# Kernel optimization log

Hardware: AMD Instinct MI355X
Metric: run time of the kernel (lower is better)

## Reference

```python
import jax, jax.numpy as jnp
import numpy as np

N = 50000       # num nodes
E = 800000      # num edges (avg degree 16)
D_IN = 128
D_H = 128
D_LAT = 64
BN_EPS = 1e-5


def _glorot(key, fan_in, fan_out):
    return jax.random.normal(key, (fan_in, fan_out), jnp.float32) / np.sqrt(fan_in).astype(np.float32)


def setup_inputs() -> dict:
    key = jax.random.key(0)
    ks = jax.random.split(key, 8)
    x = jax.random.normal(ks[0], (N, D_IN), jnp.float32)
    edge_index = jax.random.randint(ks[1], (2, E), 0, N)  # row 0 = src, row 1 = dst
    return {
        "x": x,
        "edge_index": edge_index,
        "W0": _glorot(ks[2], D_IN, D_H),
        "W1": _glorot(ks[3], D_H, D_H),
        "W_mu": _glorot(ks[4], D_H, D_LAT),
        "W_logvar": _glorot(ks[5], D_H, D_LAT),
        "gamma0": jnp.ones((D_H,), jnp.float32),
        "beta0": jnp.zeros((D_H,), jnp.float32),
        "gamma1": jnp.ones((D_H,), jnp.float32),
        "beta1": jnp.zeros((D_H,), jnp.float32),
    }


def _gcn_conv(h, W, src, dst, dinv):
    # Standard GCN with self-loops: D^{-1/2}(A+I)D^{-1/2} (X W)
    m = h @ W                                   # [N, out]
    coef = (dinv[src] * dinv[dst])[:, None]     # [E, 1]
    out = jax.ops.segment_sum(m[src] * coef, dst, num_segments=N)
    return out + m * (dinv * dinv)[:, None]     # self-loop contribution


def _batchnorm(h, gamma, beta):
    mean = jnp.mean(h, axis=0)
    var = jnp.var(h, axis=0)
    return (h - mean) * jax.lax.rsqrt(var + BN_EPS) * gamma + beta


def reference(x, edge_index, W0, W1, W_mu, W_logvar, gamma0, beta0, gamma1, beta1):
    # decoder_type='graph', augment_type=None, used_edge_weight=False,
    # use_FCencoder=False, num_domains=1; dropout is identity in reference.
    src, dst = edge_index[0], edge_index[1]
    deg = jax.ops.segment_sum(jnp.ones((E,), x.dtype), dst, num_segments=N) + 1.0
    dinv = jax.lax.rsqrt(deg)

    h = _gcn_conv(x, W0, src, dst, dinv)
    h = jax.nn.relu(_batchnorm(h, gamma0, beta0))
    h = _gcn_conv(h, W1, src, dst, dinv)
    h = jax.nn.relu(_batchnorm(h, gamma1, beta1))

    z_mean = _gcn_conv(h, W_mu, src, dst, dinv)
    z_log_std = _gcn_conv(h, W_logvar, src, dst, dinv)
    return (z_mean, z_log_std)
```

## Files before the change

kernel.cpp:

```cpp
#include <hip/hip_runtime.h>
#include <hip/hip_bf16.h>


using short8 = __attribute__((ext_vector_type(8))) short;
using f32x4  = __attribute__((ext_vector_type(4))) float;

static __device__ __forceinline__ unsigned short f2bf(float f) {
    __hip_bfloat16 h = __float2bfloat16(f);
    return *reinterpret_cast<unsigned short*>(&h);
}
static __device__ __forceinline__ float bf_lo(unsigned int u) {
    return __uint_as_float(u << 16);
}
static __device__ __forceinline__ float bf_hi(unsigned int u) {
    return __uint_as_float(u & 0xffff0000u);
}
static __device__ __forceinline__ float bf2f(unsigned short u) {
    return __uint_as_float((unsigned int)u << 16);
}

__global__ __launch_bounds__(256)
void deg_count(const int* __restrict__ ei, int* __restrict__ cnt, int E_) {
    int e = blockIdx.x * 256 + threadIdx.x;
    if (e < E_) atomicAdd(&cnt[ei[E_ + e]], 1);
}

__global__ __launch_bounds__(1024)
void scan_blocks(const int* __restrict__ cnt, float* __restrict__ dinv,
                 int* __restrict__ rowptr, int* __restrict__ partials, int n) {
    __shared__ int ls[1024];
    int tid = threadIdx.x;
    int i = blockIdx.x * 1024 + tid;
    int v = (i < n) ? cnt[i] : 0;
    if (i < n) dinv[i] = rsqrtf((float)v + 1.0f);
    ls[tid] = v;
    __syncthreads();
    #pragma unroll
    for (int off = 1; off < 1024; off <<= 1) {
        int t = (tid >= off) ? ls[tid - off] : 0;
        __syncthreads();
        ls[tid] += t;
        __syncthreads();
    }
    if (i < n) rowptr[i] = ls[tid] - v;
    if (tid == 1023) partials[blockIdx.x] = ls[1023];
}

__global__ __launch_bounds__(1024)
void scan_partials(int* __restrict__ partials, int* __restrict__ rowptr_n,
                   int nb) {
    __shared__ int ls[1024];
    int tid = threadIdx.x;
    int v = (tid < nb) ? partials[tid] : 0;
    ls[tid] = v;
    __syncthreads();
    #pragma unroll
    for (int off = 1; off < 1024; off <<= 1) {
        int t = (tid >= off) ? ls[tid - off] : 0;
        __syncthreads();
        ls[tid] += t;
        __syncthreads();
    }
    if (tid < nb) partials[tid] = ls[tid] - v;
    if (tid == 1023) *rowptr_n = ls[1023];
}

__global__ __launch_bounds__(256)
void scan_add(int* __restrict__ rowptr, int* __restrict__ gcursor,
              const int* __restrict__ partials, int n) {
    int i = blockIdx.x * 256 + threadIdx.x;
    if (i < n) {
        int v = rowptr[i] + partials[i >> 10];
        rowptr[i] = v;
        if ((i & 127) == 0) gcursor[i >> 7] = v;
    }
}

#define BCHUNK 4096
__global__ __launch_bounds__(256)
void bin_edges(const int* __restrict__ ei, const float* __restrict__ dinv,
               int* __restrict__ gcursor, uint2* __restrict__ binned, int E_) {
    __shared__ int hist[512];
    __shared__ int gbase[512];
    __shared__ int cur[512];
    const int tid = threadIdx.x;
    const int e0 = blockIdx.x * BCHUNK;

    #pragma unroll
    for (int q = 0; q < 2; ++q) hist[q * 256 + tid] = 0;
    __syncthreads();

    for (int i = tid; i < BCHUNK; i += 256) {
        int e = e0 + i;
        if (e < E_) atomicAdd(&hist[ei[E_ + e] >> 7], 1);
    }
    __syncthreads();

    #pragma unroll
    for (int q = 0; q < 2; ++q) {
        int b = q * 256 + tid;
        int c = hist[b];
        gbase[b] = c ? atomicAdd(&gcursor[b], c) : 0;
        cur[b] = 0;
    }
    __syncthreads();

    for (int i = tid; i < BCHUNK; i += 256) {
        int e = e0 + i;
        if (e >= E_) continue;
        int s = ei[e], d = ei[E_ + e];
        float coef = dinv[s] * dinv[d];
        unsigned int cb = (__float_as_uint(coef) + 0x8000u) >> 16;
        unsigned int entry = ((unsigned int)s << 15) | (cb & 0x7fffu);
        int b = d >> 7;
        int p = gbase[b] + atomicAdd(&cur[b], 1);
        binned[p] = make_uint2(entry, (unsigned int)(d & 127));
    }
}

__global__ __launch_bounds__(256)
void place_edges(const uint2* __restrict__ binned, const int* __restrict__ rowptr,
                 unsigned int* __restrict__ csr, int n) {
    __shared__ int cur[128];
    const int tid = threadIdx.x;
    const int n0 = blockIdx.x * 128;
    const int nn = min(128, n - n0);
    if (tid < nn) cur[tid] = rowptr[n0 + tid];
    __syncthreads();
    const int beg = rowptr[n0];
    const int end = rowptr[min(n0 + 128, n)];
    for (int i = beg + tid; i < end; i += 256) {
        uint2 v = binned[i];
        int p = atomicAdd(&cur[v.y], 1);
        csr[p] = v.x;
    }
}

template<bool XBF, bool FUSE_BN, bool SPLIT_W>
__global__ __launch_bounds__(256)
void gemm_mfma(const void* __restrict__ Xv, const float* __restrict__ Wa,
               const float* __restrict__ Wb, const float* __restrict__ sc,
               const float* __restrict__ sh, unsigned short* __restrict__ Y,
               int nRows) {
    __shared__ unsigned short wt[128 * 128];

    const int tid = threadIdx.x;

    #pragma unroll
    for (int it = 0; it < 16; ++it) {
        int flat4 = it * 256 + tid;
        int k  = flat4 >> 5;
        int c0 = (flat4 & 31) * 4;
        const float* srcp;
        if (!SPLIT_W) srcp = Wa + k * 128 + c0;
        else          srcp = (c0 < 64) ? (Wa + k * 64 + c0)
                                       : (Wb + k * 64 + (c0 - 64));
        float4 v = *(const float4*)srcp;
        float vv[4] = {v.x, v.y, v.z, v.w};
        #pragma unroll
        for (int j = 0; j < 4; ++j) {
            int c = c0 + j;
            wt[c * 128 + (k ^ ((c & 7) << 3))] = f2bf(vv[j]);
        }
    }
    __syncthreads();

    const int lane = tid & 63;
    const int wv   = tid >> 6;
    const int lm   = lane & 15;
    const int lg   = lane >> 4;
    const int row0 = blockIdx.x * 128 + wv * 32;

    f32x4 acc[2][8] = {};

    #pragma unroll
    for (int ks = 0; ks < 4; ++ks) {
        const int k0 = ks * 32 + lg * 8;

        short8 a[2];
        #pragma unroll
        for (int mf = 0; mf < 2; ++mf) {
            int r = row0 + mf * 16 + lm;
            if (r < nRows) {
                if (XBF) {
                    a[mf] = *(const short8*)((const unsigned short*)Xv +
                                             (size_t)r * 128 + k0);
                    if (FUSE_BN) {
                        float4 s0 = *(const float4*)(sc + k0);
                        float4 s1 = *(const float4*)(sc + k0 + 4);
                        float4 h0 = *(const float4*)(sh + k0);
                        float4 h1 = *(const float4*)(sh + k0 + 4);
                        float sv[8] = {s0.x, s0.y, s0.z, s0.w, s1.x, s1.y, s1.z, s1.w};
                        float hv[8] = {h0.x, h0.y, h0.z, h0.w, h1.x, h1.y, h1.z, h1.w};
                        #pragma unroll
                        for (int j = 0; j < 8; ++j) {
                            float v = bf2f((unsigned short)a[mf][j]);
                            v = fmaxf(v * sv[j] + hv[j], 0.f);
                            a[mf][j] = (short)f2bf(v);
                        }
                    }
                } else {
                    const float* xp = (const float*)Xv + (size_t)r * 128 + k0;
                    float4 p0 = *(const float4*)xp;
                    float4 p1 = *(const float4*)(xp + 4);
                    float pv[8] = {p0.x, p0.y, p0.z, p0.w, p1.x, p1.y, p1.z, p1.w};
                    #pragma unroll
                    for (int j = 0; j < 8; ++j) a[mf][j] = (short)f2bf(pv[j]);
                }
            } else {
                a[mf] = short8{};
            }
        }

        #pragma unroll
        for (int f = 0; f < 8; ++f) {
            int c = f * 16 + lm;
            short8 b = *(const short8*)&wt[c * 128 + (k0 ^ ((c & 7) << 3))];
            acc[0][f] = __builtin_amdgcn_mfma_f32_16x16x32_bf16(a[0], b, acc[0][f], 0, 0, 0);
            acc[1][f] = __builtin_amdgcn_mfma_f32_16x16x32_bf16(a[1], b, acc[1][f], 0, 0, 0);
        }
    }

    #pragma unroll
    for (int mf = 0; mf < 2; ++mf) {
        #pragma unroll
        for (int reg = 0; reg < 4; ++reg) {
            int r = row0 + mf * 16 + lg * 4 + reg;
            if (r >= nRows) continue;
            #pragma unroll
            for (int f = 0; f < 8; ++f)
                Y[(size_t)r * 128 + f * 16 + lm] = f2bf(acc[mf][f][reg]);
        }
    }
}

template<bool TO_OUT>
__global__ __launch_bounds__(256)
void gather_bf(const unsigned short* __restrict__ M,
               const int* __restrict__ rowptr,
               const unsigned int* __restrict__ csr,
               const float* __restrict__ dinv, void* __restrict__ O, int n) {
    int wid  = (blockIdx.x * 256 + threadIdx.x) >> 6;
    int lane = threadIdx.x & 63;
    if (wid >= n) return;
    const unsigned int* m2 = (const unsigned int*)M;

    float di = dinv[wid];
    unsigned int su = m2[(size_t)wid * 64 + lane];
    float c = di * di;
    float ax0 = bf_lo(su) * c, ay0 = bf_hi(su) * c;
    float ax1 = 0.f, ay1 = 0.f, ax2 = 0.f, ay2 = 0.f, ax3 = 0.f, ay3 = 0.f;
    float ax4 = 0.f, ay4 = 0.f, ax5 = 0.f, ay5 = 0.f, ax6 = 0.f, ay6 = 0.f;
    float ax7 = 0.f, ay7 = 0.f;

    int beg = __builtin_amdgcn_readfirstlane(rowptr[wid]);
    int end = __builtin_amdgcn_readfirstlane(rowptr[wid + 1]);

    int k = beg;
    for (; k + 7 < end; k += 8) {
        unsigned int e0 = csr[k],     e1 = csr[k + 1];
        unsigned int e2 = csr[k + 2], e3 = csr[k + 3];
        unsigned int e4 = csr[k + 4], e5 = csr[k + 5];
        unsigned int e6 = csr[k + 6], e7 = csr[k + 7];
        unsigned int u0 = m2[(size_t)(e0 >> 15) * 64 + lane];
        unsigned int u1 = m2[(size_t)(e1 >> 15) * 64 + lane];
        unsigned int u2 = m2[(size_t)(e2 >> 15) * 64 + lane];
        unsigned int u3 = m2[(size_t)(e3 >> 15) * 64 + lane];
        unsigned int u4 = m2[(size_t)(e4 >> 15) * 64 + lane];
        unsigned int u5 = m2[(size_t)(e5 >> 15) * 64 + lane];
        unsigned int u6 = m2[(size_t)(e6 >> 15) * 64 + lane];
        unsigned int u7 = m2[(size_t)(e7 >> 15) * 64 + lane];
        float w0 = __uint_as_float((e0 & 0x7fffu) << 16);
        float w1 = __uint_as_float((e1 & 0x7fffu) << 16);
        float w2 = __uint_as_float((e2 & 0x7fffu) << 16);
        float w3 = __uint_as_float((e3 & 0x7fffu) << 16);
        float w4 = __uint_as_float((e4 & 0x7fffu) << 16);
        float w5 = __uint_as_float((e5 & 0x7fffu) << 16);
        float w6 = __uint_as_float((e6 & 0x7fffu) << 16);
        float w7 = __uint_as_float((e7 & 0x7fffu) << 16);
        ax0 += w0 * bf_lo(u0); ay0 += w0 * bf_hi(u0);
        ax1 += w1 * bf_lo(u1); ay1 += w1 * bf_hi(u1);
        ax2 += w2 * bf_lo(u2); ay2 += w2 * bf_hi(u2);
        ax3 += w3 * bf_lo(u3); ay3 += w3 * bf_hi(u3);
        ax4 += w4 * bf_lo(u4); ay4 += w4 * bf_hi(u4);
        ax5 += w5 * bf_lo(u5); ay5 += w5 * bf_hi(u5);
        ax6 += w6 * bf_lo(u6); ay6 += w6 * bf_hi(u6);
        ax7 += w7 * bf_lo(u7); ay7 += w7 * bf_hi(u7);
    }
    for (; k < end; ++k) {
        unsigned int e0 = csr[k];
        unsigned int u0 = m2[(size_t)(e0 >> 15) * 64 + lane];
        float w0 = __uint_as_float((e0 & 0x7fffu) << 16);
        ax0 += w0 * bf_lo(u0); ay0 += w0 * bf_hi(u0);
    }
    float ax = ((ax0 + ax1) + (ax2 + ax3)) + ((ax4 + ax5) + (ax6 + ax7));
    float ay = ((ay0 + ay1) + (ay2 + ay3)) + ((ay4 + ay5) + (ay6 + ay7));

    if (!TO_OUT) {
        unsigned int o = (unsigned int)f2bf(ax) | ((unsigned int)f2bf(ay) << 16);
        ((unsigned int*)O)[(size_t)wid * 64 + lane] = o;
    } else {
        float* Of = (float*)O;
        float* dst = (lane < 32)
            ? Of + (size_t)wid * 64 + 2 * lane
            : Of + (size_t)n * 64 + (size_t)wid * 64 + 2 * (lane - 32);
        *(float2*)dst = make_float2(ax, ay);
    }
}

__global__ __launch_bounds__(256)
void bn_stats(const unsigned short* __restrict__ H, float* __restrict__ stats,
              const float* __restrict__ gamma, const float* __restrict__ beta,
              float* __restrict__ sc, float* __restrict__ sh,
              unsigned int* __restrict__ ticket, int n) {
    const uint4* h4 = (const uint4*)H;
    const int tid = threadIdx.x;
    const int cg = tid & 15;
    const int rg = tid >> 4;
    float s[8] = {}, q[8] = {};
    for (int r = blockIdx.x * 16 + rg; r < n; r += gridDim.x * 16) {
        uint4 u = h4[(size_t)r * 16 + cg];
        float v[8] = {bf_lo(u.x), bf_hi(u.x), bf_lo(u.y), bf_hi(u.y),
                      bf_lo(u.z), bf_hi(u.z), bf_lo(u.w), bf_hi(u.w)};
        #pragma unroll
        for (int j = 0; j < 8; ++j) { s[j] += v[j]; q[j] += v[j] * v[j]; }
    }
    __shared__ float ls[256][17];
    #pragma unroll
    for (int j = 0; j < 8; ++j) { ls[tid][j] = s[j]; ls[tid][8 + j] = q[j]; }
    __syncthreads();
    if (tid < 128) {
        int cgrp = tid >> 3, j = tid & 7;
        float S = 0.f, Q = 0.f;
        #pragma unroll
        for (int g = 0; g < 16; ++g) {
            S += ls[(g << 4) | cgrp][j];
            Q += ls[(g << 4) | cgrp][8 + j];
        }
        atomicAdd(&stats[tid], S);
        atomicAdd(&stats[128 + tid], Q);
    }
    __syncthreads();
    __shared__ int lastFlag;
    if (tid == 0) {
        __threadfence();
        unsigned int t = atomicAdd(ticket, 1u);
        lastFlag = (t == gridDim.x - 1);
    }
    __syncthreads();
    if (lastFlag && tid < 128) {
        float Ssum = __hip_atomic_load(&stats[tid], __ATOMIC_RELAXED,
                                       __HIP_MEMORY_SCOPE_AGENT);
        float Qsum = __hip_atomic_load(&stats[128 + tid], __ATOMIC_RELAXED,
                                       __HIP_MEMORY_SCOPE_AGENT);
        float inv_n = 1.0f / (float)n;
        float mean = Ssum * inv_n;
        float var  = Qsum * inv_n - mean * mean;
        float sv = rsqrtf(var + 1e-5f) * gamma[tid];
        sc[tid] = sv;
        sh[tid] = beta[tid] - mean * sv;
    }
}

extern "C" void kernel_launch(void* const* d_in, const int* in_sizes, int n_in,
                              void* d_out, int out_size, void* d_ws, size_t ws_size,
                              hipStream_t stream) {
    const float* x    = (const float*)d_in[0];
    const int*   ei   = (const int*)d_in[1];
    const float* W0   = (const float*)d_in[2];
    const float* W1   = (const float*)d_in[3];
    const float* Wmu  = (const float*)d_in[4];
    const float* Wlog = (const float*)d_in[5];
    const float* g0   = (const float*)d_in[6];
    const float* b0   = (const float*)d_in[7];
    const float* g1   = (const float*)d_in[8];
    const float* b1   = (const float*)d_in[9];

    const int N_ = in_sizes[0] / 128;
    const int E_ = in_sizes[1] / 2;
    float* out = (float*)d_out;

    char* w = (char*)d_ws;
    auto carve = [&](size_t bytes) {
        char* p = w;
        w += (bytes + 255) & ~(size_t)255;
        return p;
    };
    int*   cnt     = (int*)  carve((size_t)N_ * 4);
    float* stats0  = (float*)carve(256 * 4);
    float* stats1  = (float*)carve(256 * 4);
    unsigned int* ticket0 = (unsigned int*)carve(256);
    unsigned int* ticket1 = (unsigned int*)carve(256);
    char*  zend    = w;
    float* dinv    = (float*)carve((size_t)N_ * 4);
    int*   rowptr  = (int*)  carve((size_t)(N_ + 1) * 4);
    int*   gcursor = (int*)  carve(512 * 4);
    int*   partials= (int*)  carve(1024 * 4);
    unsigned int* csr = (unsigned int*)carve((size_t)E_ * 4);
    uint2* binned  = (uint2*)carve((size_t)E_ * 8);
    float* sc0     = (float*)carve(128 * 4);
    float* sh0     = (float*)carve(128 * 4);
    float* sc1     = (float*)carve(128 * 4);
    float* sh1     = (float*)carve(128 * 4);
    unsigned short* Mbf = (unsigned short*)carve((size_t)N_ * 128 * 2);
    unsigned short* Hb  = (unsigned short*)carve((size_t)N_ * 128 * 2);

    const int gGemm = (N_ + 127) / 128;
    const int gGath = (N_ * 64 + 255) / 256;
    const int nb    = (N_ + 1023) / 1024;
    const int nbk   = (N_ + 127) / 128;
    const int gBin  = (E_ + BCHUNK - 1) / BCHUNK;

    hipMemsetAsync(cnt, 0, (size_t)(zend - (char*)cnt), stream);
    deg_count<<<(E_ + 255) / 256, 256, 0, stream>>>(ei, cnt, E_);
    scan_blocks<<<nb, 1024, 0, stream>>>(cnt, dinv, rowptr, partials, N_);
    scan_partials<<<1, 1024, 0, stream>>>(partials, rowptr + N_, nb);
    scan_add<<<(N_ + 255) / 256, 256, 0, stream>>>(rowptr, gcursor, partials, N_);
    bin_edges<<<gBin, 256, 0, stream>>>(ei, dinv, gcursor, binned, E_);
    place_edges<<<nbk, 256, 0, stream>>>(binned, rowptr, csr, N_);

    gemm_mfma<false, false, false><<<gGemm, 256, 0, stream>>>(
        x, W0, nullptr, nullptr, nullptr, Mbf, N_);
    gather_bf<false><<<gGath, 256, 0, stream>>>(Mbf, rowptr, csr, dinv, Hb, N_);
    bn_stats<<<512, 256, 0, stream>>>(Hb, stats0, g0, b0, sc0, sh0, ticket0, N_);

    gemm_mfma<true, true, false><<<gGemm, 256, 0, stream>>>(
        Hb, W1, nullptr, sc0, sh0, Mbf, N_);
    gather_bf<false><<<gGath, 256, 0, stream>>>(Mbf, rowptr, csr, dinv, Hb, N_);
    bn_stats<<<512, 256, 0, stream>>>(Hb, stats1, g1, b1, sc1, sh1, ticket1, N_);

    gemm_mfma<true, true, true><<<gGemm, 256, 0, stream>>>(
        Hb, Wmu, Wlog, sc1, sh1, Mbf, N_);
    gather_bf<true><<<gGath, 256, 0, stream>>>(Mbf, rowptr, csr, dinv, out, N_);
}
```

Measured before the change: 259.8 us.

## Fuse BatchNorm statistics into gather kernel with sharded atomic accumulators

Merges the bn_stats pass into the aggregation kernel: each block reduces sum and sum-of-squares of its 4 rows in shared memory and atomically adds them into one of 16 shadow stat buffers, and the last block to finish folds these into scale and shift. This avoids re-reading the hidden activations and removes two launches. The cost is 12500 blocks each issuing 256 float atomics, contended across only 16 buffers, and a statistics order that is no longer deterministic. deg_count is also changed to read destinations as int4 with four atomics per thread.

```diff
diff --git a/kernel.cpp b/kernel.cpp
--- a/kernel.cpp
+++ b/kernel.cpp
@@ -21,8 +21,15 @@
 
 __global__ __launch_bounds__(256)
 void deg_count(const int* __restrict__ ei, int* __restrict__ cnt, int E_) {
-    int e = blockIdx.x * 256 + threadIdx.x;
-    if (e < E_) atomicAdd(&cnt[ei[E_ + e]], 1);
+    int i = blockIdx.x * 256 + threadIdx.x;
+    int nq = E_ >> 2;
+    const int4* d4 = (const int4*)(ei + E_);
+    if (i < nq) {
+        int4 v = d4[i];
+        atomicAdd(&cnt[v.x], 1); atomicAdd(&cnt[v.y], 1);
+        atomicAdd(&cnt[v.z], 1); atomicAdd(&cnt[v.w], 1);
+    }
+    if (i < (E_ & 3)) atomicAdd(&cnt[ei[E_ + nq * 4 + i]], 1);
 }
 
 __global__ __launch_bounds__(1024)
@@ -234,28 +241,12 @@
     }
 }
 
-template<bool TO_OUT>
-__global__ __launch_bounds__(256)
-void gather_bf(const unsigned short* __restrict__ M,
-               const int* __restrict__ rowptr,
-               const unsigned int* __restrict__ csr,
-               const float* __restrict__ dinv, void* __restrict__ O, int n) {
-    int wid  = (blockIdx.x * 256 + threadIdx.x) >> 6;
-    int lane = threadIdx.x & 63;
-    if (wid >= n) return;
-    const unsigned int* m2 = (const unsigned int*)M;
-
-    float di = dinv[wid];
-    unsigned int su = m2[(size_t)wid * 64 + lane];
-    float c = di * di;
-    float ax0 = bf_lo(su) * c, ay0 = bf_hi(su) * c;
+static __device__ __forceinline__ void gather_row(
+        const unsigned int* __restrict__ m2, const unsigned int* __restrict__ csr,
+        int beg, int end, int lane, float& ax, float& ay) {
     float ax1 = 0.f, ay1 = 0.f, ax2 = 0.f, ay2 = 0.f, ax3 = 0.f, ay3 = 0.f;
     float ax4 = 0.f, ay4 = 0.f, ax5 = 0.f, ay5 = 0.f, ax6 = 0.f, ay6 = 0.f;
     float ax7 = 0.f, ay7 = 0.f;
-
-    int beg = __builtin_amdgcn_readfirstlane(rowptr[wid]);
-    int end = __builtin_amdgcn_readfirstlane(rowptr[wid + 1]);
-
     int k = beg;
     for (; k + 7 < end; k += 8) {
         unsigned int e0 = csr[k],     e1 = csr[k + 1];
@@ -278,7 +269,7 @@
         float w5 = __uint_as_float((e5 & 0x7fffu) << 16);
         float w6 = __uint_as_float((e6 & 0x7fffu) << 16);
         float w7 = __uint_as_float((e7 & 0x7fffu) << 16);
-        ax0 += w0 * bf_lo(u0); ay0 += w0 * bf_hi(u0);
+        ax  += w0 * bf_lo(u0); ay  += w0 * bf_hi(u0);
         ax1 += w1 * bf_lo(u1); ay1 += w1 * bf_hi(u1);
         ax2 += w2 * bf_lo(u2); ay2 += w2 * bf_hi(u2);
         ax3 += w3 * bf_lo(u3); ay3 += w3 * bf_hi(u3);
@@ -291,54 +282,56 @@
         unsigned int e0 = csr[k];
         unsigned int u0 = m2[(size_t)(e0 >> 15) * 64 + lane];
         float w0 = __uint_as_float((e0 & 0x7fffu) << 16);
-        ax0 += w0 * bf_lo(u0); ay0 += w0 * bf_hi(u0);
-    }
-    float ax = ((ax0 + ax1) + (ax2 + ax3)) + ((ax4 + ax5) + (ax6 + ax7));
-    float ay = ((ay0 + ay1) + (ay2 + ay3)) + ((ay4 + ay5) + (ay6 + ay7));
-
-    if (!TO_OUT) {
+        ax += w0 * bf_lo(u0); ay += w0 * bf_hi(u0);
+    }
+    ax = ((ax + ax1) + (ax2 + ax3)) + ((ax4 + ax5) + (ax6 + ax7));
+    ay = ((ay + ay1) + (ay2 + ay3)) + ((ay4 + ay5) + (ay6 + ay7));
+}
+
+__global__ __launch_bounds__(256)
+void gather_stats(const unsigned short* __restrict__ M,
+                  const int* __restrict__ rowptr,
+                  const unsigned int* __restrict__ csr,
+                  const float* __restrict__ dinv, unsigned int* __restrict__ O,
+                  float* __restrict__ stats,
+                  const float* __restrict__ gamma, const float* __restrict__ beta,
+                  float* __restrict__ sc, float* __restrict__ sh,
+                  unsigned int* __restrict__ ticket, int n) {
+    const int tid  = threadIdx.x;
+    const int wv   = tid >> 6;
+    const int lane = tid & 63;
+    const int wid  = blockIdx.x * 4 + wv;
+    const unsigned int* m2 = (const unsigned int*)M;
+
+    float ax = 0.f, ay = 0.f;
+    if (wid < n) {
+        float di = dinv[wid];
+        unsigned int su = m2[(size_t)wid * 64 + lane];
+        float c = di * di;
+        ax = bf_lo(su) * c; ay = bf_hi(su) * c;
+        int beg = __builtin_amdgcn_readfirstlane(rowptr[wid]);
+        int end = __builtin_amdgcn_readfirstlane(rowptr[wid + 1]);
+        gather_row(m2, csr, beg, end, lane, ax, ay);
         unsigned int o = (unsigned int)f2bf(ax) | ((unsigned int)f2bf(ay) << 16);
-        ((unsigned int*)O)[(size_t)wid * 64 + lane] = o;
-    } else {
-        float* Of = (float*)O;
-        float* dst = (lane < 32)
-            ? Of + (size_t)wid * 64 + 2 * lane
-            : Of + (size_t)n * 64 + (size_t)wid * 64 + 2 * (lane - 32);
-        *(float2*)dst = make_float2(ax, ay);
-    }
-}
-
-__global__ __launch_bounds__(256)
-void bn_stats(const unsigned short* __restrict__ H, float* __restrict__ stats,
-              const float* __restrict__ gamma, const float* __restrict__ beta,
-              float* __restrict__ sc, float* __restrict__ sh,
-              unsigned int* __restrict__ ticket, int n) {
-    const uint4* h4 = (const uint4*)H;
-    const int tid = threadIdx.x;
-    const int cg = tid & 15;
-    const int rg = tid >> 4;
-    float s[8] = {}, q[8] = {};
-    for (int r = blockIdx.x * 16 + rg; r < n; r += gridDim.x * 16) {
-        uint4 u = h4[(size_t)r * 16 + cg];
-        float v[8] = {bf_lo(u.x), bf_hi(u.x), bf_lo(u.y), bf_hi(u.y),
-                      bf_lo(u.z), bf_hi(u.z), bf_lo(u.w), bf_hi(u.w)};
-        #pragma unroll
-        for (int j = 0; j < 8; ++j) { s[j] += v[j]; q[j] += v[j] * v[j]; }
-    }
-    __shared__ float ls[256][17];
-    #pragma unroll
-    for (int j = 0; j < 8; ++j) { ls[tid][j] = s[j]; ls[tid][8 + j] = q[j]; }
-    __syncthreads();
-    if (tid < 128) {
-        int cgrp = tid >> 3, j = tid & 7;
-        float S = 0.f, Q = 0.f;
-        #pragma unroll
-        for (int g = 0; g < 16; ++g) {
-            S += ls[(g << 4) | cgrp][j];
-            Q += ls[(g << 4) | cgrp][8 + j];
-        }
-        atomicAdd(&stats[tid], S);
-        atomicAdd(&stats[128 + tid], Q);
+        O[(size_t)wid * 64 + lane] = o;
+    }
+
+    __shared__ float ls[4][64][4];
+    ls[wv][lane][0] = ax;       ls[wv][lane][1] = ay;
+    ls[wv][lane][2] = ax * ax;  ls[wv][lane][3] = ay * ay;
+    __syncthreads();
+    if (tid < 64) {
+        float sx = 0.f, sy = 0.f, qx = 0.f, qy = 0.f;
+        #pragma unroll
+        for (int g = 0; g < 4; ++g) {
+            sx += ls[g][tid][0]; sy += ls[g][tid][1];
+            qx += ls[g][tid][2]; qy += ls[g][tid][3];
+        }
+        float* shadow = stats + (blockIdx.x & 15) * 256;
+        atomicAdd(&shadow[2 * tid],       sx);
+        atomicAdd(&shadow[2 * tid + 1],   sy);
+        atomicAdd(&shadow[128 + 2 * tid], qx);
+        atomicAdd(&shadow[129 + 2 * tid], qy);
     }
     __syncthreads();
     __shared__ int lastFlag;
@@ -349,17 +342,46 @@
     }
     __syncthreads();
     if (lastFlag && tid < 128) {
-        float Ssum = __hip_atomic_load(&stats[tid], __ATOMIC_RELAXED,
-                                       __HIP_MEMORY_SCOPE_AGENT);
-        float Qsum = __hip_atomic_load(&stats[128 + tid], __ATOMIC_RELAXED,
-                                       __HIP_MEMORY_SCOPE_AGENT);
+        float S = 0.f, Q = 0.f;
+        #pragma unroll
+        for (int g = 0; g < 16; ++g) {
+            S += __hip_atomic_load(&stats[g * 256 + tid], __ATOMIC_RELAXED,
+                                   __HIP_MEMORY_SCOPE_AGENT);
+            Q += __hip_atomic_load(&stats[g * 256 + 128 + tid], __ATOMIC_RELAXED,
+                                   __HIP_MEMORY_SCOPE_AGENT);
+        }
         float inv_n = 1.0f / (float)n;
-        float mean = Ssum * inv_n;
-        float var  = Qsum * inv_n - mean * mean;
+        float mean = S * inv_n;
+        float var  = Q * inv_n - mean * mean;
         float sv = rsqrtf(var + 1e-5f) * gamma[tid];
         sc[tid] = sv;
         sh[tid] = beta[tid] - mean * sv;
     }
+}
+
+__global__ __launch_bounds__(256)
+void gather_out(const unsigned short* __restrict__ M,
+                const int* __restrict__ rowptr,
+                const unsigned int* __restrict__ csr,
+                const float* __restrict__ dinv, float* __restrict__ O, int n) {
+    int wid  = (blockIdx.x * 256 + threadIdx.x) >> 6;
+    int lane = threadIdx.x & 63;
+    if (wid >= n) return;
+    const unsigned int* m2 = (const unsigned int*)M;
+
+    float di = dinv[wid];
+    unsigned int su = m2[(size_t)wid * 64 + lane];
+    float c = di * di;
+    float ax = bf_lo(su) * c, ay = bf_hi(su) * c;
+
+    int beg = __builtin_amdgcn_readfirstlane(rowptr[wid]);
+    int end = __builtin_amdgcn_readfirstlane(rowptr[wid + 1]);
+    gather_row(m2, csr, beg, end, lane, ax, ay);
+
+    float* dst = (lane < 32)
+        ? O + (size_t)wid * 64 + 2 * lane
+        : O + (size_t)n * 64 + (size_t)wid * 64 + 2 * (lane - 32);
+    *(float2*)dst = make_float2(ax, ay);
 }
 
 extern "C" void kernel_launch(void* const* d_in, const int* in_sizes, int n_in,
@@ -387,8 +409,8 @@
         return p;
     };
     int*   cnt     = (int*)  carve((size_t)N_ * 4);
-    float* stats0  = (float*)carve(256 * 4);
-    float* stats1  = (float*)carve(256 * 4);
+    float* stats0  = (float*)carve(16 * 256 * 4);
+    float* stats1  = (float*)carve(16 * 256 * 4);
     unsigned int* ticket0 = (unsigned int*)carve(256);
     unsigned int* ticket1 = (unsigned int*)carve(256);
     char*  zend    = w;
@@ -406,13 +428,13 @@
     unsigned short* Hb  = (unsigned short*)carve((size_t)N_ * 128 * 2);
 
     const int gGemm = (N_ + 127) / 128;
-    const int gGath = (N_ * 64 + 255) / 256;
+    const int gGath = (N_ + 3) / 4;
     const int nb    = (N_ + 1023) / 1024;
     const int nbk   = (N_ + 127) / 128;
     const int gBin  = (E_ + BCHUNK - 1) / BCHUNK;
 
     hipMemsetAsync(cnt, 0, (size_t)(zend - (char*)cnt), stream);
-    deg_count<<<(E_ + 255) / 256, 256, 0, stream>>>(ei, cnt, E_);
+    deg_count<<<((E_ >> 2) + 255) / 256, 256, 0, stream>>>(ei, cnt, E_);
     scan_blocks<<<nb, 1024, 0, stream>>>(cnt, dinv, rowptr, partials, N_);
     scan_partials<<<1, 1024, 0, stream>>>(partials, rowptr + N_, nb);
     scan_add<<<(N_ + 255) / 256, 256, 0, stream>>>(rowptr, gcursor, partials, N_);
@@ -421,15 +443,16 @@
 
     gemm_mfma<false, false, false><<<gGemm, 256, 0, stream>>>(
         x, W0, nullptr, nullptr, nullptr, Mbf, N_);
-    gather_bf<false><<<gGath, 256, 0, stream>>>(Mbf, rowptr, csr, dinv, Hb, N_);
-    bn_stats<<<512, 256, 0, stream>>>(Hb, stats0, g0, b0, sc0, sh0, ticket0, N_);
+    gather_stats<<<gGath, 256, 0, stream>>>(Mbf, rowptr, csr, dinv,
+        (unsigned int*)Hb, stats0, g0, b0, sc0, sh0, ticket0, N_);
 
     gemm_mfma<true, true, false><<<gGemm, 256, 0, stream>>>(
         Hb, W1, nullptr, sc0, sh0, Mbf, N_);
-    gather_bf<false><<<gGath, 256, 0, stream>>>(Mbf, rowptr, csr, dinv, Hb, N_);
-    bn_stats<<<512, 256, 0, stream>>>(Hb, stats1, g1, b1, sc1, sh1, ticket1, N_);
+    gather_stats<<<gGath, 256, 0, stream>>>(Mbf, rowptr, csr, dinv,
+        (unsigned int*)Hb, stats1, g1, b1, sc1, sh1, ticket1, N_);
 
     gemm_mfma<true, true, true><<<gGemm, 256, 0, stream>>>(
         Hb, Wmu, Wlog, sc1, sh1, Mbf, N_);
-    gather_bf<true><<<gGath, 256, 0, stream>>>(Mbf, rowptr, csr, dinv, out, N_);
-}
+    gather_out<<<(N_ * 64 + 255) / 256, 256, 0, stream>>>(
+        Mbf, rowptr, csr, dinv, out, N_);
+}
```

New measurement: 885.3 us. 241% more time.
